# Optimization experiments

Hardware: AMD Instinct MI355X
Metric: run time of the kernel (lower is better)

## Reference

```python
import jax, jax.numpy as jnp
import numpy as np

N = 10000       # num_nodes
E = 1000        # num_hyperedges
STEPS = 30      # horizon


def setup_inputs() -> dict:
    key = jax.random.key(0)
    k1, k2 = jax.random.split(key, 2)
    infected0 = jax.random.uniform(k1, (N,)) < 0.01
    x = jnp.stack([(~infected0).astype(jnp.float32),
                   infected0.astype(jnp.float32),
                   jnp.zeros((N,), jnp.float32)], axis=1)
    H = (jax.random.uniform(k2, (STEPS - 1, E, N)) < 0.001).astype(jnp.float32)
    beta = jnp.full((N,), 0.01, jnp.float32)
    gamma = jnp.full((N,), 0.038, jnp.float32)
    return {"x": x, "H": H, "beta": beta, "gamma": gamma, "steps": STEPS}


def _simulate(x, H, beta, gamma):
    n = x.shape[0]
    key0 = jax.random.key(42)

    def step(carry, H_t):
        p_prev, s_prev, key = carry
        key, k1, k2 = jax.random.split(key, 3)
        infected = s_prev[:, 1]
        # hypergraph Laplacian step: H_t.T @ (H_t @ infected)
        new_cases = beta * (H_t.T @ (H_t @ infected))
        new_rec = gamma * infected
        p = jnp.stack([p_prev[:, 0] - new_cases,
                       p_prev[:, 1] + new_cases - new_rec,
                       p_prev[:, 2] + new_rec], axis=1)
        p = jnp.clip(p, 0.0, 1.0)
        # per-node stochastic SIR state transitions (vectorized)
        u1 = jax.random.uniform(k1, (n,))
        u2 = jax.random.uniform(k2, (n,))
        was_S = s_prev[:, 0] == 1
        was_I = s_prev[:, 1] == 1
        s_to_I = was_S & (u1 < p[:, 1])
        i_event = was_I & (u1 < p[:, 2])
        i_to_R = i_event & (u2 < 0.5)
        i_to_S = i_event & ~(u2 < 0.5)
        new_S = (was_S & ~s_to_I) | i_to_S
        new_I = s_to_I | (was_I & ~i_event)
        new_R = (~was_S & ~was_I) | i_to_R
        s = jnp.stack([new_S, new_I, new_R], axis=1).astype(x.dtype)
        return (p, s, key), (p, s)

    (_, _, _), (p_seq, s_seq) = jax.lax.scan(step, (x, x, key0), H)
    pathogen = jnp.concatenate([x[None], p_seq], axis=0)    # (steps, N, 3)
    state = jnp.concatenate([x[None], s_seq], axis=0)       # (steps, N, 3)
    return pathogen, state


def reference(x, H, beta, gamma, steps):
    # steps == H.shape[0] + 1 by construction
    return _simulate(x, H, beta, gamma)
```

## Files before the change

### kernel.cpp

```cpp
#include <hip/hip_runtime.h>
#include <stdint.h>

constexpr int NN = 10000;
constexpr int EE = 1000;
constexpr int TT = 30;
constexpr int TS = TT - 1;
constexpr int ROW = NN * 3;
constexpr int S_OFF = TT * ROW;
constexpr int CAP_E = 48;
constexpr int WPR = CAP_E / 2;
constexpr int PREW = 8;
constexpr int SIMT = 1024;
constexpr int NPT  = 10;

__host__ __device__ inline void tf2x32(uint32_t k0, uint32_t k1,
                                       uint32_t x0, uint32_t x1,
                                       uint32_t &o0, uint32_t &o1) {
  uint32_t ks2 = k0 ^ k1 ^ 0x1BD11BDAu;
  x0 += k0; x1 += k1;
#define TFR(r) do { x0 += x1; x1 = (x1 << (r)) | (x1 >> (32 - (r))); x1 ^= x0; } while (0)
  TFR(13); TFR(15); TFR(26); TFR(6);
  x0 += k1;  x1 += ks2 + 1u;
  TFR(17); TFR(29); TFR(16); TFR(24);
  x0 += ks2; x1 += k0 + 2u;
  TFR(13); TFR(15); TFR(26); TFR(6);
  x0 += k0;  x1 += k1 + 3u;
  TFR(17); TFR(29); TFR(16); TFR(24);
  x0 += k1;  x1 += ks2 + 4u;
  TFR(13); TFR(15); TFR(26); TFR(6);
  x0 += ks2; x1 += k0 + 5u;
#undef TFR
  o0 = x0; o1 = x1;
}

__device__ inline float bits_to_uniform(uint32_t bits) {
  float f = __uint_as_float((bits >> 9) | 0x3F800000u) - 1.0f;
  return f < 0.f ? 0.f : f;
}

struct StepKeys { uint32_t k1a[TS], k1b[TS], k2a[TS], k2b[TS]; };

__device__ inline void bar_lds() {
  asm volatile("s_waitcnt lgkmcnt(0)\n\ts_barrier" ::: "memory");
}

__global__ void k_rand(float* __restrict__ u1, float* __restrict__ u2, StepKeys keys) {
  int t = blockIdx.y;
  int n = blockIdx.x * blockDim.x + threadIdx.x;
  if (n >= NN) return;
  uint32_t a, b;
  tf2x32(keys.k1a[t], keys.k1b[t], 0u, (uint32_t)n, a, b);
  u1[t * NN + n] = bits_to_uniform(a ^ b);
  tf2x32(keys.k2a[t], keys.k2b[t], 0u, (uint32_t)n, a, b);
  u2[t * NN + n] = bits_to_uniform(a ^ b);
}

__global__ void k_scan(const float* __restrict__ H, int* __restrict__ edge_cnt,
                       uint32_t* __restrict__ edge_words) {
  const int row = blockIdx.x;
  const int t = row / EE;
  const int e = row - t * EE;
  __shared__ int cnt;
  __shared__ uint16_t list[CAP_E];
  if (threadIdx.x == 0) cnt = 0;
  __syncthreads();
  const float4* hrow = reinterpret_cast<const float4*>(H + (size_t)row * NN);
  for (int i = threadIdx.x; i < NN / 4; i += blockDim.x) {
    float4 v = hrow[i];
    int b4 = i * 4;
    if (v.x != 0.f) { int p = atomicAdd(&cnt, 1); if (p < CAP_E) list[p] = (uint16_t)(b4 + 0); }
    if (v.y != 0.f) { int p = atomicAdd(&cnt, 1); if (p < CAP_E) list[p] = (uint16_t)(b4 + 1); }
    if (v.z != 0.f) { int p = atomicAdd(&cnt, 1); if (p < CAP_E) list[p] = (uint16_t)(b4 + 2); }
    if (v.w != 0.f) { int p = atomicAdd(&cnt, 1); if (p < CAP_E) list[p] = (uint16_t)(b4 + 3); }
  }
  __syncthreads();
  int c = cnt < CAP_E ? cnt : CAP_E;
  if (threadIdx.x == 0) edge_cnt[row] = c;
  int words = (c + 1) >> 1;
  int wmax = words > PREW ? words : PREW;
  if ((int)threadIdx.x < wmax) {
    int j = threadIdx.x;
    uint32_t lo = (2 * j     < c) ? (uint32_t)list[2 * j]     : 0xFFFFu;
    uint32_t hi = (2 * j + 1 < c) ? (uint32_t)list[2 * j + 1] : 0xFFFFu;
    edge_words[((size_t)t * WPR + j) * EE + e] = lo | (hi << 16);
  }
}

__global__ __launch_bounds__(SIMT, 4)
void k_sim(float* __restrict__ out, const float* __restrict__ x,
           const int* __restrict__ edge_cnt, const uint32_t* __restrict__ edge_words,
           const float* __restrict__ u1, const float* __restrict__ u2,
           const float* __restrict__ beta, const float* __restrict__ gamma_) {
  __shared__ uint8_t s_st[NN];
  __shared__ int nv[NN];
  const int tid = threadIdx.x;

  float p0[NPT], p1[NPT], p2[NPT], bet[NPT], gam[NPT];
#pragma unroll
  for (int k = 0; k < NPT; ++k) {
    int n = tid + k * SIMT;
    if (n < NN) {
      float x0 = x[n * 3 + 0], x1 = x[n * 3 + 1], x2 = x[n * 3 + 2];
      p0[k] = x0; p1[k] = x1; p2[k] = x2;
      s_st[n] = (x1 == 1.f) ? 1 : ((x0 == 1.f) ? 0 : 2);
      nv[n] = 0;
      bet[k] = beta[n]; gam[k] = gamma_[n];
      out[n * 3 + 0] = x0; out[n * 3 + 1] = x1; out[n * 3 + 2] = x2;
      out[S_OFF + n * 3 + 0] = x0; out[S_OFF + n * 3 + 1] = x1; out[S_OFF + n * 3 + 2] = x2;
    }
  }
  bar_lds();

  for (int t = 0; t < TS; ++t) {
    float u1r[NPT], u2r[NPT];
#pragma unroll
    for (int k = 0; k < NPT; ++k) {
      int n = tid + k * SIMT;
      if (n < NN) { u1r[k] = u1[(size_t)t * NN + n]; u2r[k] = u2[(size_t)t * NN + n]; }
    }

    if (tid < EE) {
      const uint32_t* wb = edge_words + (size_t)t * WPR * EE + tid;
      int ec = edge_cnt[t * EE + tid]; if (ec > CAP_E) ec = CAP_E;
      uint32_t w[PREW];
#pragma unroll
      for (int j = 0; j < PREW; ++j) w[j] = wb[(size_t)j * EE];
      int words = (ec + 1) >> 1;
      int s = 0;
#pragma unroll
      for (int j = 0; j < PREW; ++j) {
        uint32_t lo = w[j] & 0xFFFFu, hi = w[j] >> 16;
        if (lo != 0xFFFFu) s += (s_st[lo] == 1) ? 1 : 0;
        if (hi != 0xFFFFu) s += (s_st[hi] == 1) ? 1 : 0;
      }
      for (int j = PREW; j < words; ++j) {
        uint32_t ww = wb[(size_t)j * EE];
        uint32_t lo = ww & 0xFFFFu, hi = ww >> 16;
        if (lo != 0xFFFFu) s += (s_st[lo] == 1) ? 1 : 0;
        if (hi != 0xFFFFu) s += (s_st[hi] == 1) ? 1 : 0;
      }
      if (s > 0) {
#pragma unroll
        for (int j = 0; j < PREW; ++j) {
          uint32_t lo = w[j] & 0xFFFFu, hi = w[j] >> 16;
          if (lo != 0xFFFFu) atomicAdd(&nv[lo], s);
          if (hi != 0xFFFFu) atomicAdd(&nv[hi], s);
        }
        for (int j = PREW; j < words; ++j) {
          uint32_t ww = wb[(size_t)j * EE];
          uint32_t lo = ww & 0xFFFFu, hi = ww >> 16;
          if (lo != 0xFFFFu) atomicAdd(&nv[lo], s);
          if (hi != 0xFFFFu) atomicAdd(&nv[hi], s);
        }
      }
    }
    bar_lds();

    float* po = out + (size_t)(t + 1) * ROW;
    float* so = out + S_OFF + (size_t)(t + 1) * ROW;
#pragma unroll
    for (int k = 0; k < NPT; ++k) {
      int n = tid + k * SIMT;
      if (n < NN) {
        int st = s_st[n];
        int v = nv[n];
        nv[n] = 0;
        float s1 = (st == 1) ? 1.f : 0.f;
        float new_cases = __fmul_rn(bet[k], (float)v);
        float new_rec   = __fmul_rn(gam[k], s1);
        float q0 = fminf(1.f, fmaxf(0.f, __fsub_rn(p0[k], new_cases)));
        float q1 = fminf(1.f, fmaxf(0.f, __fsub_rn(__fadd_rn(p1[k], new_cases), new_rec)));
        float q2 = fminf(1.f, fmaxf(0.f, __fadd_rn(p2[k], new_rec)));
        p0[k] = q0; p1[k] = q1; p2[k] = q2;

        bool was_S  = (st == 0);
        bool was_I  = (st == 1);
        bool s_to_I = was_S && (u1r[k] < q1);
        bool i_event = was_I && (u1r[k] < q2);
        bool u2lt   = (u2r[k] < 0.5f);
        bool i_to_R = i_event && u2lt;
        bool i_to_S = i_event && !u2lt;
        bool new_S = (was_S && !s_to_I) || i_to_S;
        bool new_I = s_to_I || (was_I && !i_event);
        bool new_R = (!was_S && !was_I) || i_to_R;

        po[n * 3 + 0] = q0; po[n * 3 + 1] = q1; po[n * 3 + 2] = q2;
        so[n * 3 + 0] = new_S ? 1.f : 0.f;
        so[n * 3 + 1] = new_I ? 1.f : 0.f;
        so[n * 3 + 2] = new_R ? 1.f : 0.f;
        s_st[n] = new_I ? 1 : (new_S ? 0 : 2);
      }
    }
    bar_lds();
  }
}

extern "C" void kernel_launch(void* const* d_in, const int* in_sizes, int n_in,
                              void* d_out, int out_size, void* d_ws, size_t ws_size,
                              hipStream_t stream) {
  const float* x      = (const float*)d_in[0];
  const float* H      = (const float*)d_in[1];
  const float* beta   = (const float*)d_in[2];
  const float* gamma_ = (const float*)d_in[3];
  float* out = (float*)d_out;

  StepKeys keys;
  uint32_t key0 = 0u, key1 = 42u;
  for (int t = 0; t < TS; ++t) {
    uint32_t a0, b0, a1, b1, a2, b2;
    tf2x32(key0, key1, 0u, 0u, a0, b0);
    tf2x32(key0, key1, 0u, 1u, a1, b1);
    tf2x32(key0, key1, 0u, 2u, a2, b2);
    keys.k1a[t] = a1; keys.k1b[t] = b1; keys.k2a[t] = a2; keys.k2b[t] = b2;
    key0 = a0; key1 = b0;
  }

  size_t off = 0;
  auto take = [&](size_t bytes) { size_t o = off; off += (bytes + 255) & ~(size_t)255; return o; };
  size_t o_ec = take((size_t)TS * EE * sizeof(int));
  size_t o_ew = take((size_t)TS * WPR * EE * sizeof(uint32_t));
  size_t o_u1 = take((size_t)TS * NN * sizeof(float));
  size_t o_u2 = take((size_t)TS * NN * sizeof(float));

  int*      edge_cnt   = (int*)((char*)d_ws + o_ec);
  uint32_t* edge_words = (uint32_t*)((char*)d_ws + o_ew);
  float*    u1         = (float*)((char*)d_ws + o_u1);
  float*    u2         = (float*)((char*)d_ws + o_u2);

  k_rand<<<dim3((NN + 255) / 256, TS), 256, 0, stream>>>(u1, u2, keys);
  k_scan<<<TS * EE, 256, 0, stream>>>(H, edge_cnt, edge_words);
  k_sim<<<1, SIMT, 0, stream>>>(out, x, edge_cnt, edge_words, u1, u2, beta, gamma_);
}
```

Baseline: 1.754 ms.

## Fuse RNG into scan kernel and give sim threads contiguous vectorized node blocks

```diff
diff --git a/kernel.cpp b/kernel.cpp
--- a/kernel.cpp
+++ b/kernel.cpp
@@ -10,8 +10,9 @@
 constexpr int CAP_E = 48;
 constexpr int WPR = CAP_E / 2;
 constexpr int PREW = 8;
-constexpr int SIMT = 1024;
-constexpr int NPT  = 10;
+constexpr int SIMT = 512;
+constexpr int NPT  = 20;
+constexpr int RB   = (NN + 255) / 256;
 
 __host__ __device__ inline void tf2x32(uint32_t k0, uint32_t k1,
                                        uint32_t x0, uint32_t x1,
@@ -44,22 +45,25 @@
   asm volatile("s_waitcnt lgkmcnt(0)\n\ts_barrier" ::: "memory");
 }
 
-__global__ void k_rand(float* __restrict__ u1, float* __restrict__ u2, StepKeys keys) {
-  int t = blockIdx.y;
-  int n = blockIdx.x * blockDim.x + threadIdx.x;
-  if (n >= NN) return;
-  uint32_t a, b;
-  tf2x32(keys.k1a[t], keys.k1b[t], 0u, (uint32_t)n, a, b);
-  u1[t * NN + n] = bits_to_uniform(a ^ b);
-  tf2x32(keys.k2a[t], keys.k2b[t], 0u, (uint32_t)n, a, b);
-  u2[t * NN + n] = bits_to_uniform(a ^ b);
-}
-
-__global__ void k_scan(const float* __restrict__ H, int* __restrict__ edge_cnt,
-                       uint32_t* __restrict__ edge_words) {
+__global__ void k_scanrand(const float* __restrict__ H, int* __restrict__ edge_cnt,
+                           uint32_t* __restrict__ edge_words,
+                           float* __restrict__ u1, float* __restrict__ u2, StepKeys keys) {
   const int row = blockIdx.x;
   const int t = row / EE;
   const int e = row - t * EE;
+
+  if (row < TS * RB) {
+    int rt = row / RB, chunk = row - rt * RB;
+    int n = chunk * 256 + threadIdx.x;
+    if (n < NN) {
+      uint32_t a, b;
+      tf2x32(keys.k1a[rt], keys.k1b[rt], 0u, (uint32_t)n, a, b);
+      u1[rt * NN + n] = bits_to_uniform(a ^ b);
+      tf2x32(keys.k2a[rt], keys.k2b[rt], 0u, (uint32_t)n, a, b);
+      u2[rt * NN + n] = bits_to_uniform(a ^ b);
+    }
+  }
+
   __shared__ int cnt;
   __shared__ uint16_t list[CAP_E];
   if (threadIdx.x == 0) cnt = 0;
@@ -86,7 +90,7 @@
   }
 }
 
-__global__ __launch_bounds__(SIMT, 4)
+__global__ __launch_bounds__(SIMT, 2)
 void k_sim(float* __restrict__ out, const float* __restrict__ x,
            const int* __restrict__ edge_cnt, const uint32_t* __restrict__ edge_words,
            const float* __restrict__ u1, const float* __restrict__ u2,
@@ -94,37 +98,81 @@
   __shared__ uint8_t s_st[NN];
   __shared__ int nv[NN];
   const int tid = threadIdx.x;
+  const bool owner = (tid < NN / NPT);
+  const int n0 = tid * NPT;
 
   float p0[NPT], p1[NPT], p2[NPT], bet[NPT], gam[NPT];
-#pragma unroll
-  for (int k = 0; k < NPT; ++k) {
-    int n = tid + k * SIMT;
-    if (n < NN) {
-      float x0 = x[n * 3 + 0], x1 = x[n * 3 + 1], x2 = x[n * 3 + 2];
-      p0[k] = x0; p1[k] = x1; p2[k] = x2;
-      s_st[n] = (x1 == 1.f) ? 1 : ((x0 == 1.f) ? 0 : 2);
-      nv[n] = 0;
-      bet[k] = beta[n]; gam[k] = gamma_[n];
-      out[n * 3 + 0] = x0; out[n * 3 + 1] = x1; out[n * 3 + 2] = x2;
-      out[S_OFF + n * 3 + 0] = x0; out[S_OFF + n * 3 + 1] = x1; out[S_OFF + n * 3 + 2] = x2;
-    }
+  if (owner) {
+    const float4* xv = reinterpret_cast<const float4*>(x + (size_t)n0 * 3);
+    float4* o0v = reinterpret_cast<float4*>(out + (size_t)n0 * 3);
+    float4* o1v = reinterpret_cast<float4*>(out + S_OFF + (size_t)n0 * 3);
+#pragma unroll
+    for (int j = 0; j < NPT * 3 / 4; ++j) {
+      float4 v = xv[j];
+      o0v[j] = v; o1v[j] = v;
+      reinterpret_cast<float4*>(p0)[0] = v;
+    }
+    const float4* bv = reinterpret_cast<const float4*>(beta + n0);
+    const float4* gv = reinterpret_cast<const float4*>(gamma_ + n0);
+#pragma unroll
+    for (int j = 0; j < NPT / 4; ++j) {
+      reinterpret_cast<float4*>(bet)[j] = bv[j];
+      reinterpret_cast<float4*>(gam)[j] = gv[j];
+    }
+    uint32_t codes[NPT / 4];
+#pragma unroll
+    for (int k = 0; k < NPT; ++k) {
+      int n = n0 + k;
+      float x0 = x[n * 3 + 0], x1 = x[n * 3 + 1];
+      p0[k] = x0; p1[k] = x1; p2[k] = x[n * 3 + 2];
+      uint32_t c = (x1 == 1.f) ? 1u : ((x0 == 1.f) ? 0u : 2u);
+      if ((k & 3) == 0) codes[k >> 2] = c; else codes[k >> 2] |= c << (8 * (k & 3));
+    }
+#pragma unroll
+    for (int j = 0; j < NPT / 4; ++j)
+      reinterpret_cast<uint32_t*>(s_st + n0)[j] = codes[j];
+    int4 z = make_int4(0, 0, 0, 0);
+#pragma unroll
+    for (int j = 0; j < NPT / 4; ++j)
+      reinterpret_cast<int4*>(nv + n0)[j] = z;
   }
   bar_lds();
 
   for (int t = 0; t < TS; ++t) {
     float u1r[NPT], u2r[NPT];
-#pragma unroll
-    for (int k = 0; k < NPT; ++k) {
-      int n = tid + k * SIMT;
-      if (n < NN) { u1r[k] = u1[(size_t)t * NN + n]; u2r[k] = u2[(size_t)t * NN + n]; }
-    }
-
-    if (tid < EE) {
-      const uint32_t* wb = edge_words + (size_t)t * WPR * EE + tid;
-      int ec = edge_cnt[t * EE + tid]; if (ec > CAP_E) ec = CAP_E;
-      uint32_t w[PREW];
-#pragma unroll
-      for (int j = 0; j < PREW; ++j) w[j] = wb[(size_t)j * EE];
+    if (owner) {
+      const float4* u1v = reinterpret_cast<const float4*>(u1 + (size_t)t * NN + n0);
+      const float4* u2v = reinterpret_cast<const float4*>(u2 + (size_t)t * NN + n0);
+#pragma unroll
+      for (int j = 0; j < NPT / 4; ++j) {
+        reinterpret_cast<float4*>(u1r)[j] = u1v[j];
+        reinterpret_cast<float4*>(u2r)[j] = u2v[j];
+      }
+    }
+
+    uint32_t w0[PREW], w1[PREW];
+    int ec0 = 0, ec1 = 0;
+    const int e1i = tid + SIMT;
+    {
+      const uint32_t* wb0 = edge_words + (size_t)t * WPR * EE + tid;
+      ec0 = edge_cnt[t * EE + tid];
+#pragma unroll
+      for (int j = 0; j < PREW; ++j) w0[j] = wb0[(size_t)j * EE];
+      if (e1i < EE) {
+        const uint32_t* wb1 = edge_words + (size_t)t * WPR * EE + e1i;
+        ec1 = edge_cnt[t * EE + e1i];
+#pragma unroll
+        for (int j = 0; j < PREW; ++j) w1[j] = wb1[(size_t)j * EE];
+      }
+    }
+#pragma unroll
+    for (int pass = 0; pass < 2; ++pass) {
+      int e = pass == 0 ? tid : e1i;
+      if (e >= EE) continue;
+      int ec = pass == 0 ? ec0 : ec1;
+      if (ec > CAP_E) ec = CAP_E;
+      const uint32_t* w = pass == 0 ? w0 : w1;
+      const uint32_t* wb = edge_words + (size_t)t * WPR * EE + e;
       int words = (ec + 1) >> 1;
       int s = 0;
 #pragma unroll
@@ -156,17 +204,27 @@
     }
     bar_lds();
 
-    float* po = out + (size_t)(t + 1) * ROW;
-    float* so = out + S_OFF + (size_t)(t + 1) * ROW;
-#pragma unroll
-    for (int k = 0; k < NPT; ++k) {
-      int n = tid + k * SIMT;
-      if (n < NN) {
-        int st = s_st[n];
-        int v = nv[n];
-        nv[n] = 0;
+    if (owner) {
+      float* po = out + (size_t)(t + 1) * ROW + (size_t)n0 * 3;
+      float* so = out + S_OFF + (size_t)(t + 1) * ROW + (size_t)n0 * 3;
+      int nvr[NPT];
+      uint32_t str[NPT / 4];
+#pragma unroll
+      for (int j = 0; j < NPT / 4; ++j) {
+        reinterpret_cast<int4*>(nvr)[j] = reinterpret_cast<const int4*>(nv + n0)[j];
+        str[j] = reinterpret_cast<const uint32_t*>(s_st + n0)[j];
+      }
+      int4 z = make_int4(0, 0, 0, 0);
+#pragma unroll
+      for (int j = 0; j < NPT / 4; ++j)
+        reinterpret_cast<int4*>(nv + n0)[j] = z;
+      uint32_t newc[NPT / 4];
+      float pst[12], sst[12];
+#pragma unroll
+      for (int k = 0; k < NPT; ++k) {
+        int st = (str[k >> 2] >> (8 * (k & 3))) & 0xFFu;
         float s1 = (st == 1) ? 1.f : 0.f;
-        float new_cases = __fmul_rn(bet[k], (float)v);
+        float new_cases = __fmul_rn(bet[k], (float)nvr[k]);
         float new_rec   = __fmul_rn(gam[k], s1);
         float q0 = fminf(1.f, fmaxf(0.f, __fsub_rn(p0[k], new_cases)));
         float q1 = fminf(1.f, fmaxf(0.f, __fsub_rn(__fadd_rn(p1[k], new_cases), new_rec)));
@@ -183,13 +241,28 @@
         bool new_S = (was_S && !s_to_I) || i_to_S;
         bool new_I = s_to_I || (was_I && !i_event);
         bool new_R = (!was_S && !was_I) || i_to_R;
-
-        po[n * 3 + 0] = q0; po[n * 3 + 1] = q1; po[n * 3 + 2] = q2;
-        so[n * 3 + 0] = new_S ? 1.f : 0.f;
-        so[n * 3 + 1] = new_I ? 1.f : 0.f;
-        so[n * 3 + 2] = new_R ? 1.f : 0.f;
-        s_st[n] = new_I ? 1 : (new_S ? 0 : 2);
-      }
+        uint32_t c = new_I ? 1u : (new_S ? 0u : 2u);
+        if ((k & 3) == 0) newc[k >> 2] = c; else newc[k >> 2] |= c << (8 * (k & 3));
+
+        int kk = k & 3;
+        pst[kk * 3 + 0] = q0; pst[kk * 3 + 1] = q1; pst[kk * 3 + 2] = q2;
+        sst[kk * 3 + 0] = new_S ? 1.f : 0.f;
+        sst[kk * 3 + 1] = new_I ? 1.f : 0.f;
+        sst[kk * 3 + 2] = new_R ? 1.f : 0.f;
+        if (kk == 3) {
+          int g = k >> 2;
+          float4* pv = reinterpret_cast<float4*>(po + g * 12);
+          float4* sv = reinterpret_cast<float4*>(so + g * 12);
+#pragma unroll
+          for (int j = 0; j < 3; ++j) {
+            pv[j] = reinterpret_cast<float4*>(pst)[j];
+            sv[j] = reinterpret_cast<float4*>(sst)[j];
+          }
+        }
+      }
+#pragma unroll
+      for (int j = 0; j < NPT / 4; ++j)
+        reinterpret_cast<uint32_t*>(s_st + n0)[j] = newc[j];
     }
     bar_lds();
   }
@@ -227,7 +300,6 @@
   float*    u1         = (float*)((char*)d_ws + o_u1);
   float*    u2         = (float*)((char*)d_ws + o_u2);
 
-  k_rand<<<dim3((NN + 255) / 256, TS), 256, 0, stream>>>(u1, u2, keys);
-  k_scan<<<TS * EE, 256, 0, stream>>>(H, edge_cnt, edge_words);
+  k_scanrand<<<TS * EE, 256, 0, stream>>>(H, edge_cnt, edge_words, u1, u2, keys);
   k_sim<<<1, SIMT, 0, stream>>>(out, x, edge_cnt, edge_words, u1, u2, beta, gamma_);
 }
```

Measured after the change: 1.971 ms. 12.4% more time.

## Fuse RNG, incidence scan and simulation into one producer-consumer kernel

Applied to the files above, without the earlier changes.

```diff
diff --git a/kernel.cpp b/kernel.cpp
--- a/kernel.cpp
+++ b/kernel.cpp
@@ -12,6 +12,7 @@
 constexpr int PREW = 8;
 constexpr int SIMT = 1024;
 constexpr int NPT  = 10;
+constexpr int RBLK = (NN + SIMT - 1) / SIMT;
 
 __host__ __device__ inline void tf2x32(uint32_t k0, uint32_t k1,
                                        uint32_t x0, uint32_t x1,
@@ -44,56 +45,77 @@
   asm volatile("s_waitcnt lgkmcnt(0)\n\ts_barrier" ::: "memory");
 }
 
-__global__ void k_rand(float* __restrict__ u1, float* __restrict__ u2, StepKeys keys) {
-  int t = blockIdx.y;
-  int n = blockIdx.x * blockDim.x + threadIdx.x;
-  if (n >= NN) return;
-  uint32_t a, b;
-  tf2x32(keys.k1a[t], keys.k1b[t], 0u, (uint32_t)n, a, b);
-  u1[t * NN + n] = bits_to_uniform(a ^ b);
-  tf2x32(keys.k2a[t], keys.k2b[t], 0u, (uint32_t)n, a, b);
-  u2[t * NN + n] = bits_to_uniform(a ^ b);
-}
-
-__global__ void k_scan(const float* __restrict__ H, int* __restrict__ edge_cnt,
-                       uint32_t* __restrict__ edge_words) {
-  const int row = blockIdx.x;
-  const int t = row / EE;
-  const int e = row - t * EE;
-  __shared__ int cnt;
-  __shared__ uint16_t list[CAP_E];
-  if (threadIdx.x == 0) cnt = 0;
-  __syncthreads();
-  const float4* hrow = reinterpret_cast<const float4*>(H + (size_t)row * NN);
-  for (int i = threadIdx.x; i < NN / 4; i += blockDim.x) {
-    float4 v = hrow[i];
-    int b4 = i * 4;
-    if (v.x != 0.f) { int p = atomicAdd(&cnt, 1); if (p < CAP_E) list[p] = (uint16_t)(b4 + 0); }
-    if (v.y != 0.f) { int p = atomicAdd(&cnt, 1); if (p < CAP_E) list[p] = (uint16_t)(b4 + 1); }
-    if (v.z != 0.f) { int p = atomicAdd(&cnt, 1); if (p < CAP_E) list[p] = (uint16_t)(b4 + 2); }
-    if (v.w != 0.f) { int p = atomicAdd(&cnt, 1); if (p < CAP_E) list[p] = (uint16_t)(b4 + 3); }
-  }
-  __syncthreads();
-  int c = cnt < CAP_E ? cnt : CAP_E;
-  if (threadIdx.x == 0) edge_cnt[row] = c;
-  int words = (c + 1) >> 1;
-  int wmax = words > PREW ? words : PREW;
-  if ((int)threadIdx.x < wmax) {
-    int j = threadIdx.x;
-    uint32_t lo = (2 * j     < c) ? (uint32_t)list[2 * j]     : 0xFFFFu;
-    uint32_t hi = (2 * j + 1 < c) ? (uint32_t)list[2 * j + 1] : 0xFFFFu;
-    edge_words[((size_t)t * WPR + j) * EE + e] = lo | (hi << 16);
-  }
+#define ALD(p)    __hip_atomic_load((p),  __ATOMIC_RELAXED, __HIP_MEMORY_SCOPE_AGENT)
+#define AST(p, v) __hip_atomic_store((p), (v), __ATOMIC_RELAXED, __HIP_MEMORY_SCOPE_AGENT)
+
+__global__ void k_zero(unsigned* __restrict__ cnt) {
+  if (threadIdx.x < TS) cnt[threadIdx.x] = 0u;
 }
 
 __global__ __launch_bounds__(SIMT, 4)
-void k_sim(float* __restrict__ out, const float* __restrict__ x,
-           const int* __restrict__ edge_cnt, const uint32_t* __restrict__ edge_words,
-           const float* __restrict__ u1, const float* __restrict__ u2,
-           const float* __restrict__ beta, const float* __restrict__ gamma_) {
-  __shared__ uint8_t s_st[NN];
-  __shared__ int nv[NN];
+void k_fused(const float* __restrict__ H,
+             int* __restrict__ edge_cnt, uint32_t* __restrict__ edge_words,
+             unsigned long long* __restrict__ uv, unsigned* __restrict__ cnt,
+             const float* __restrict__ x,
+             const float* __restrict__ beta, const float* __restrict__ gamma_,
+             float* __restrict__ out, StepKeys keys) {
   const int tid = threadIdx.x;
+
+  if (blockIdx.x > 0) {
+    const int row = blockIdx.x - 1;
+    const int t = row / EE;
+    const int e = row - t * EE;
+
+    if (e < RBLK) {
+      int n = e * SIMT + tid;
+      if (n < NN) {
+        uint32_t a, b;
+        tf2x32(keys.k1a[t], keys.k1b[t], 0u, (uint32_t)n, a, b);
+        uint32_t b1 = __float_as_uint(bits_to_uniform(a ^ b));
+        tf2x32(keys.k2a[t], keys.k2b[t], 0u, (uint32_t)n, a, b);
+        uint32_t b2 = __float_as_uint(bits_to_uniform(a ^ b));
+        unsigned long long raw = (unsigned long long)b1 | ((unsigned long long)b2 << 32);
+        AST(&uv[(size_t)t * NN + n], raw);
+      }
+    }
+
+    __shared__ int scnt;
+    __shared__ uint16_t list[CAP_E];
+    if (tid == 0) scnt = 0;
+    __syncthreads();
+    const float4* hrow = reinterpret_cast<const float4*>(H + (size_t)row * NN);
+    float4 v0 = hrow[tid];
+    float4 v1 = hrow[tid + 1024];
+    float4 v2 = make_float4(0.f, 0.f, 0.f, 0.f);
+    const bool has2 = tid + 2048 < NN / 4;
+    if (has2) v2 = hrow[tid + 2048];
+#define PROC(v, b4) do { \
+    if ((v).x != 0.f) { int p = atomicAdd(&scnt, 1); if (p < CAP_E) list[p] = (uint16_t)((b4) + 0); } \
+    if ((v).y != 0.f) { int p = atomicAdd(&scnt, 1); if (p < CAP_E) list[p] = (uint16_t)((b4) + 1); } \
+    if ((v).z != 0.f) { int p = atomicAdd(&scnt, 1); if (p < CAP_E) list[p] = (uint16_t)((b4) + 2); } \
+    if ((v).w != 0.f) { int p = atomicAdd(&scnt, 1); if (p < CAP_E) list[p] = (uint16_t)((b4) + 3); } \
+  } while (0)
+    PROC(v0, 4 * tid);
+    PROC(v1, 4 * (tid + 1024));
+    if (has2) PROC(v2, 4 * (tid + 2048));
+#undef PROC
+    __syncthreads();
+    int c = scnt < CAP_E ? scnt : CAP_E;
+    if (tid == 0) AST(&edge_cnt[row], c);
+    int words = (c + 1) >> 1;
+    int wmax = words > PREW ? words : PREW;
+    if (tid < wmax) {
+      uint32_t lo = (2 * tid     < c) ? (uint32_t)list[2 * tid]     : 0xFFFFu;
+      uint32_t hi = (2 * tid + 1 < c) ? (uint32_t)list[2 * tid + 1] : 0xFFFFu;
+      AST(&edge_words[((size_t)t * WPR + tid) * EE + e], lo | (hi << 16));
+    }
+    __syncthreads();
+    if (tid == 0)
+      __hip_atomic_fetch_add(&cnt[t], 1u, __ATOMIC_RELAXED, __HIP_MEMORY_SCOPE_AGENT);
+    return;
+  }
+
+  __shared__ int nvst[NN];
 
   float p0[NPT], p1[NPT], p2[NPT], bet[NPT], gam[NPT];
 #pragma unroll
@@ -102,8 +124,8 @@
     if (n < NN) {
       float x0 = x[n * 3 + 0], x1 = x[n * 3 + 1], x2 = x[n * 3 + 2];
       p0[k] = x0; p1[k] = x1; p2[k] = x2;
-      s_st[n] = (x1 == 1.f) ? 1 : ((x0 == 1.f) ? 0 : 2);
-      nv[n] = 0;
+      int st = (x1 == 1.f) ? 1 : ((x0 == 1.f) ? 0 : 2);
+      nvst[n] = st << 16;
       bet[k] = beta[n]; gam[k] = gamma_[n];
       out[n * 3 + 0] = x0; out[n * 3 + 1] = x1; out[n * 3 + 2] = x2;
       out[S_OFF + n * 3 + 0] = x0; out[S_OFF + n * 3 + 1] = x1; out[S_OFF + n * 3 + 2] = x2;
@@ -112,59 +134,68 @@
   bar_lds();
 
   for (int t = 0; t < TS; ++t) {
+    if (tid == 0) {
+      while (ALD(&cnt[t]) < (unsigned)EE) __builtin_amdgcn_s_sleep(8);
+    }
+    bar_lds();
+
     float u1r[NPT], u2r[NPT];
-#pragma unroll
-    for (int k = 0; k < NPT; ++k) {
-      int n = tid + k * SIMT;
-      if (n < NN) { u1r[k] = u1[(size_t)t * NN + n]; u2r[k] = u2[(size_t)t * NN + n]; }
-    }
-
-    if (tid < EE) {
-      const uint32_t* wb = edge_words + (size_t)t * WPR * EE + tid;
-      int ec = edge_cnt[t * EE + tid]; if (ec > CAP_E) ec = CAP_E;
-      uint32_t w[PREW];
-#pragma unroll
-      for (int j = 0; j < PREW; ++j) w[j] = wb[(size_t)j * EE];
-      int words = (ec + 1) >> 1;
-      int s = 0;
-#pragma unroll
-      for (int j = 0; j < PREW; ++j) {
-        uint32_t lo = w[j] & 0xFFFFu, hi = w[j] >> 16;
-        if (lo != 0xFFFFu) s += (s_st[lo] == 1) ? 1 : 0;
-        if (hi != 0xFFFFu) s += (s_st[hi] == 1) ? 1 : 0;
-      }
-      for (int j = PREW; j < words; ++j) {
-        uint32_t ww = wb[(size_t)j * EE];
-        uint32_t lo = ww & 0xFFFFu, hi = ww >> 16;
-        if (lo != 0xFFFFu) s += (s_st[lo] == 1) ? 1 : 0;
-        if (hi != 0xFFFFu) s += (s_st[hi] == 1) ? 1 : 0;
-      }
-      if (s > 0) {
-#pragma unroll
-        for (int j = 0; j < PREW; ++j) {
-          uint32_t lo = w[j] & 0xFFFFu, hi = w[j] >> 16;
-          if (lo != 0xFFFFu) atomicAdd(&nv[lo], s);
-          if (hi != 0xFFFFu) atomicAdd(&nv[hi], s);
-        }
-        for (int j = PREW; j < words; ++j) {
-          uint32_t ww = wb[(size_t)j * EE];
-          uint32_t lo = ww & 0xFFFFu, hi = ww >> 16;
-          if (lo != 0xFFFFu) atomicAdd(&nv[lo], s);
-          if (hi != 0xFFFFu) atomicAdd(&nv[hi], s);
-        }
-      }
-    }
-    bar_lds();
-
-    float* po = out + (size_t)(t + 1) * ROW;
-    float* so = out + S_OFF + (size_t)(t + 1) * ROW;
 #pragma unroll
     for (int k = 0; k < NPT; ++k) {
       int n = tid + k * SIMT;
       if (n < NN) {
-        int st = s_st[n];
-        int v = nv[n];
-        nv[n] = 0;
+        unsigned long long raw = ALD(&uv[(size_t)t * NN + n]);
+        u1r[k] = __uint_as_float((uint32_t)raw);
+        u2r[k] = __uint_as_float((uint32_t)(raw >> 32));
+      }
+    }
+
+    if (tid < EE) {
+      const uint32_t* wb = edge_words + (size_t)t * WPR * EE + tid;
+      int ec = ALD(&edge_cnt[t * EE + tid]); if (ec > CAP_E) ec = CAP_E;
+      uint32_t w[PREW];
+#pragma unroll
+      for (int j = 0; j < PREW; ++j) w[j] = ALD(&wb[(size_t)j * EE]);
+      int words = (ec + 1) >> 1;
+      int s = 0;
+#pragma unroll
+      for (int j = 0; j < PREW; ++j) {
+        uint32_t lo = w[j] & 0xFFFFu, hi = w[j] >> 16;
+        if (lo != 0xFFFFu) s += ((nvst[lo] >> 16) == 1) ? 1 : 0;
+        if (hi != 0xFFFFu) s += ((nvst[hi] >> 16) == 1) ? 1 : 0;
+      }
+      for (int j = PREW; j < words; ++j) {
+        uint32_t ww = ALD(&wb[(size_t)j * EE]);
+        uint32_t lo = ww & 0xFFFFu, hi = ww >> 16;
+        if (lo != 0xFFFFu) s += ((nvst[lo] >> 16) == 1) ? 1 : 0;
+        if (hi != 0xFFFFu) s += ((nvst[hi] >> 16) == 1) ? 1 : 0;
+      }
+      if (s > 0) {
+#pragma unroll
+        for (int j = 0; j < PREW; ++j) {
+          uint32_t lo = w[j] & 0xFFFFu, hi = w[j] >> 16;
+          if (lo != 0xFFFFu) atomicAdd(&nvst[lo], s);
+          if (hi != 0xFFFFu) atomicAdd(&nvst[hi], s);
+        }
+        for (int j = PREW; j < words; ++j) {
+          uint32_t ww = ALD(&wb[(size_t)j * EE]);
+          uint32_t lo = ww & 0xFFFFu, hi = ww >> 16;
+          if (lo != 0xFFFFu) atomicAdd(&nvst[lo], s);
+          if (hi != 0xFFFFu) atomicAdd(&nvst[hi], s);
+        }
+      }
+    }
+    bar_lds();
+
+    float* po = out + (size_t)(t + 1) * ROW;
+    float* so = out + S_OFF + (size_t)(t + 1) * ROW;
+#pragma unroll
+    for (int k = 0; k < NPT; ++k) {
+      int n = tid + k * SIMT;
+      if (n < NN) {
+        int wv = nvst[n];
+        int v  = wv & 0xFFFF;
+        int st = wv >> 16;
         float s1 = (st == 1) ? 1.f : 0.f;
         float new_cases = __fmul_rn(bet[k], (float)v);
         float new_rec   = __fmul_rn(gam[k], s1);
@@ -188,10 +219,9 @@
         so[n * 3 + 0] = new_S ? 1.f : 0.f;
         so[n * 3 + 1] = new_I ? 1.f : 0.f;
         so[n * 3 + 2] = new_R ? 1.f : 0.f;
-        s_st[n] = new_I ? 1 : (new_S ? 0 : 2);
-      }
-    }
-    bar_lds();
+        nvst[n] = (new_I ? 1 : (new_S ? 0 : 2)) << 16;
+      }
+    }
   }
 }
 
@@ -219,15 +249,15 @@
   auto take = [&](size_t bytes) { size_t o = off; off += (bytes + 255) & ~(size_t)255; return o; };
   size_t o_ec = take((size_t)TS * EE * sizeof(int));
   size_t o_ew = take((size_t)TS * WPR * EE * sizeof(uint32_t));
-  size_t o_u1 = take((size_t)TS * NN * sizeof(float));
-  size_t o_u2 = take((size_t)TS * NN * sizeof(float));
+  size_t o_uv = take((size_t)TS * NN * sizeof(unsigned long long));
+  size_t o_ct = take((size_t)TS * sizeof(unsigned));
 
   int*      edge_cnt   = (int*)((char*)d_ws + o_ec);
   uint32_t* edge_words = (uint32_t*)((char*)d_ws + o_ew);
-  float*    u1         = (float*)((char*)d_ws + o_u1);
-  float*    u2         = (float*)((char*)d_ws + o_u2);
-
-  k_rand<<<dim3((NN + 255) / 256, TS), 256, 0, stream>>>(u1, u2, keys);
-  k_scan<<<TS * EE, 256, 0, stream>>>(H, edge_cnt, edge_words);
-  k_sim<<<1, SIMT, 0, stream>>>(out, x, edge_cnt, edge_words, u1, u2, beta, gamma_);
-}
+  unsigned long long* uv = (unsigned long long*)((char*)d_ws + o_uv);
+  unsigned* cnt        = (unsigned*)((char*)d_ws + o_ct);
+
+  k_zero<<<1, 64, 0, stream>>>(cnt);
+  k_fused<<<1 + TS * EE, SIMT, 0, stream>>>(H, edge_cnt, edge_words, uv, cnt,
+                                            x, beta, gamma_, out, keys);
+}
```

Result: faster. 1.605 ms (-8.5%).
